# Kernel optimization log

Measured on AMD Instinct MI355X. Metric: run time of the kernel, lower is better.

Reference implementation:

```python
import jax, jax.numpy as jnp
import numpy as np

KMEANS_ITERS = 3   # soft-kmeans refinement iterations
TOPK = 12          # hardcoded in the torch module
EPS = 1e-8


def _gather(x, idx):
    # batched_index_select: x (b, c, m); idx (b, n, k) -> (b, c, n, k)
    return jax.vmap(lambda xb, ib: xb[:, ib])(x, idx)


def _soft_kmeans(points, cent):
    # points (b, n, c); cent (b, m, c) -> refined centroids and soft assignment weights (b, n, m)
    for _ in range(KMEANS_ITERS):
        p2 = jnp.sum(points * points, axis=-1)           # (b, n)
        c2 = jnp.sum(cent * cent, axis=-1)               # (b, m)
        logits = -(p2[:, :, None] - 2.0 * jnp.einsum('bnc,bmc->bnm', points, cent) + c2[:, None, :])
        w = jax.nn.softmax(logits, axis=-1)              # (b, n, m)
        cent = jnp.einsum('bnm,bnc->bmc', w, points) / (jnp.sum(w, axis=1)[:, :, None] + EPS)
    return cent, w


def setup_inputs():
    key = jax.random.key(0)
    k1, k2, k3 = jax.random.split(key, 3)
    b, c, H, W, k = 4, 192, 80, 80, 9
    n = H * W
    out_c = 192
    x = jax.random.normal(k1, (b, c, n, 1), dtype=jnp.float32)
    edge_index = jax.random.randint(k2, (2, b, n, k), 0, n)
    conv_w = jax.random.normal(k3, (out_c, 3 * c), dtype=jnp.float32) * (1.0 / np.sqrt(3 * c))
    conv_b = jnp.zeros((out_c,), dtype=jnp.float32)
    return {"x": x, "edge_index": edge_index, "conv_w": conv_w, "conv_b": conv_b,
            "num_centroids": 50, "H": 80, "W": 80}


def reference(x, edge_index, conv_w, conv_b, num_centroids, H, W):
    b, c, n, _ = x.shape
    xs = x[..., 0]                                        # (b, c, n)
    # initial centroids: adaptive_avg_pool2d to (5, 10); H, W chosen divisible so bins are uniform
    x_img = xs.reshape(b, c, H, W)
    init_cent = x_img.reshape(b, c, 5, H // 5, 10, W // 10).mean(axis=(3, 5)).reshape(b, c, 50)
    # edge gathers + max-relative reduction
    x_i = _gather(xs, edge_index[1])                      # (b, c, n, k)
    x_j = _gather(xs, edge_index[0])                      # (b, c, n, k)
    x_j = jnp.max(x_j - x_i, axis=-1, keepdims=True)      # (b, c, n, 1)
    # soft-kmeans centroid construction
    points = jnp.transpose(xs, (0, 2, 1))                 # (b, n, c)
    cent, weights = _soft_kmeans(points, jnp.transpose(init_cent, (0, 2, 1)))
    cent = jnp.transpose(cent, (0, 2, 1))                 # (b, c, m)
    # topk centroid routing + second gather-max stage
    _, nn_idx = jax.lax.top_k(weights, TOPK)              # (b, n, 12)
    x_jc = _gather(cent, nn_idx)                          # (b, c, n, 12)
    x_jc = jnp.max(x_jc - xs[..., None], axis=-1, keepdims=True)  # (b, c, n, 1)
    # channel-interleaved concat (matches torch stack on dim=2 then reshape to 3c)
    feat = jnp.stack([x, x_j, x_jc], axis=2).reshape(b, 3 * c, n)  # (b, 3c, n)
    # BasicConv: 1x1 conv + bias + relu (norm=None)
    out = jnp.einsum('oi,bin->bon', conv_w, feat) + conv_b[None, :, None]
    return jax.nn.relu(out)[..., None]                    # (b, out_c, n, 1)
```

## Files before the change

### kernel.cpp

```cpp
#include <hip/hip_runtime.h>
#include <hip/hip_bf16.h>
#include <math.h>

#define B_   4
#define C_   192
#define N_   6400
#define K_   9
#define M_   50
#define TK_  12
#define OC_  192
#define KC_  576
#define CH_  100
#define LSTR 53
#define TSTR 72
#define XSTR 40
#define GSTR 40

typedef __bf16 b16x8 __attribute__((ext_vector_type(8)));
typedef float f32x4 __attribute__((ext_vector_type(4)));

__device__ inline unsigned short f2b(float f) {
    union { __hip_bfloat16 h; unsigned short u; } v;
    v.h = __float2bfloat16(f);
    return v.u;
}
__device__ inline float b2f(unsigned short u) {
    union { float f; unsigned int i; } v;
    v.i = ((unsigned int)u) << 16;
    return v.f;
}

__global__ void k_rearrange_w(const float* __restrict__ cw, unsigned short* __restrict__ Wg16) {
    int g = blockIdx.x * 256 + threadIdx.x;
    int o = g / KC_, r = g % KC_;
    int t = r / C_, ch = r % C_;
    Wg16[g] = f2b(cw[o * KC_ + ch * 3 + t]);
}

__global__ void k_transpose(const float* __restrict__ x, float* __restrict__ xt,
                            unsigned short* __restrict__ xt16,
                            unsigned short* __restrict__ xt16l) {
    __shared__ float tile[32][33];
    int b = blockIdx.z;
    int p0 = blockIdx.x * 32, c0 = blockIdx.y * 32;
    int tx = threadIdx.x, ty = threadIdx.y;
    const float* xb = x + (size_t)b * C_ * N_;
    float* xtb = xt + (size_t)b * N_ * C_;
    unsigned short* xt16b = xt16 + (size_t)b * N_ * C_;
    unsigned short* xt16lb = xt16l + (size_t)b * N_ * C_;
#pragma unroll
    for (int i = 0; i < 4; i++) {
        int cc = ty + 8 * i;
        tile[cc][tx] = xb[(size_t)(c0 + cc) * N_ + p0 + tx];
    }
    __syncthreads();
#pragma unroll
    for (int i = 0; i < 4; i++) {
        int pp = ty + 8 * i;
        float v = tile[tx][pp];
        size_t o = (size_t)(p0 + pp) * C_ + c0 + tx;
        xtb[o] = v;
        unsigned short hi = f2b(v);
        xt16b[o] = hi;
        xt16lb[o] = f2b(v - b2f(hi));
    }
}

__global__ __launch_bounds__(192) void k_init_cent(const float* __restrict__ xt,
        float* __restrict__ cent, float* __restrict__ c2,
        unsigned short* __restrict__ centh, unsigned short* __restrict__ centl) {
    int m = blockIdx.x, b = blockIdx.y, c = threadIdx.x;
    if (m >= M_) {
        size_t o = ((size_t)b * 64 + m) * C_ + c;
        centh[o] = 0; centl[o] = 0;
        return;
    }
    int gy = m / 10, gx = m % 10;
    const float* xtb = xt + (size_t)b * N_ * C_;
    float s = 0.f;
    for (int yy = 0; yy < 16; yy++)
        for (int xx = 0; xx < 8; xx++) {
            int p = (gy * 16 + yy) * 80 + gx * 8 + xx;
            s += xtb[(size_t)p * C_ + c];
        }
    float v = s * (1.f / 128.f);
    cent[((size_t)b * M_ + m) * C_ + c] = v;
    size_t oh = ((size_t)b * 64 + m) * C_ + c;
    unsigned short hi = f2b(v);
    centh[oh] = hi;
    centl[oh] = f2b(v - b2f(hi));
    float q = v * v;
    __shared__ float red[3];
#pragma unroll
    for (int off = 32; off > 0; off >>= 1) q += __shfl_down(q, off, 64);
    if ((c & 63) == 0) red[c >> 6] = q;
    __syncthreads();
    if (c == 0) c2[(size_t)b * M_ + m] = red[0] + red[1] + red[2];
}

__global__ __launch_bounds__(256) void k_logits_upd(const float* __restrict__ xt,
        const unsigned short* __restrict__ xt16, const unsigned short* __restrict__ xt16l,
        const float* __restrict__ cent,
        const unsigned short* __restrict__ centh, const unsigned short* __restrict__ centl,
        const float* __restrict__ c2g,
        float* __restrict__ part, float* __restrict__ wsp,
        int* __restrict__ nn, int do_topk, int fast) {
    __shared__ alignas(16) char smem[51712];
    __shared__ float sred[256];
    float* Ac = (float*)smem;
    float* Bp = (float*)(smem + 4352);
    float* lg = (float*)(smem + 20480);
    unsigned short* lgTh = (unsigned short*)smem;
    unsigned short* lgTl = (unsigned short*)(smem + 9216);
    unsigned short* xTh = (unsigned short*)(smem + 18432);
    unsigned short* xTl = (unsigned short*)(smem + 35072);
    int b = blockIdx.y;
    int blk = blockIdx.x;
    int p0 = blk * 64;
    int tid = threadIdx.x;
    int tx = tid & 15, ty = tid >> 4;
    int lr = tid >> 2, lq = tid & 3;
    int wave = tid >> 6, lane = tid & 63;
    int m16 = lane & 15, q = lane >> 4;
    const float* xb = xt + ((size_t)b * N_ + p0) * C_;
    const unsigned short* x16b = xt16 + ((size_t)b * N_ + p0) * C_;
    const unsigned short* x16lb = xt16l + ((size_t)b * N_ + p0) * C_;
    if (fast) {
        const unsigned short* chg = centh + (size_t)b * 64 * C_;
        const unsigned short* clg = centl + (size_t)b * 64 * C_;
        f32x4 acc1[4];
#pragma unroll
        for (int i = 0; i < 4; i++) acc1[i] = (f32x4){0.f, 0.f, 0.f, 0.f};
#pragma unroll
        for (int kt = 0; kt < 6; kt++) {
            int kg = kt * 32;
            size_t xo = (size_t)(wave * 16 + m16) * C_ + kg + q * 8;
            b16x8 bh = *(const b16x8*)&x16b[xo];
            b16x8 bl = *(const b16x8*)&x16lb[xo];
#pragma unroll
            for (int mt = 0; mt < 4; mt++) {
                size_t co = (size_t)(mt * 16 + m16) * C_ + kg + q * 8;
                b16x8 ah = *(const b16x8*)&chg[co];
                b16x8 al = *(const b16x8*)&clg[co];
                acc1[mt] = __builtin_amdgcn_mfma_f32_16x16x32_bf16(ah, bh, acc1[mt], 0, 0, 0);
                acc1[mt] = __builtin_amdgcn_mfma_f32_16x16x32_bf16(ah, bl, acc1[mt], 0, 0, 0);
                acc1[mt] = __builtin_amdgcn_mfma_f32_16x16x32_bf16(al, bh, acc1[mt], 0, 0, 0);
            }
        }
#pragma unroll
        for (int mt = 0; mt < 4; mt++) {
#pragma unroll
            for (int r = 0; r < 4; r++) {
                int m = mt * 16 + q * 4 + r;
                if (m < M_) {
                    float c2v = c2g[(size_t)b * M_ + m];
                    lg[(wave * 16 + m16) * LSTR + m] = 2.f * acc1[mt][r] - c2v;
                }
            }
        }
    } else {
        const float* cb = cent + (size_t)b * M_ * C_;
        float acc[4][4];
#pragma unroll
        for (int i = 0; i < 4; i++)
#pragma unroll
            for (int j = 0; j < 4; j++) acc[i][j] = 0.f;
        for (int kt = 0; kt < 12; kt++) {
            int kg = kt * 16;
            float4 cv = make_float4(0.f, 0.f, 0.f, 0.f);
            if (lr < M_) cv = *(const float4*)&cb[(size_t)lr * C_ + kg + 4 * lq];
            float4 pv = *(const float4*)&xb[(size_t)lr * C_ + kg + 4 * lq];
            __syncthreads();
            Ac[(4 * lq + 0) * 68 + lr] = cv.x; Ac[(4 * lq + 1) * 68 + lr] = cv.y;
            Ac[(4 * lq + 2) * 68 + lr] = cv.z; Ac[(4 * lq + 3) * 68 + lr] = cv.w;
            Bp[(4 * lq + 0) * 68 + lr] = pv.x; Bp[(4 * lq + 1) * 68 + lr] = pv.y;
            Bp[(4 * lq + 2) * 68 + lr] = pv.z; Bp[(4 * lq + 3) * 68 + lr] = pv.w;
            __syncthreads();
#pragma unroll
            for (int kk = 0; kk < 16; kk++) {
                float4 a = *(const float4*)&Ac[kk * 68 + 4 * ty];
                float4 bb = *(const float4*)&Bp[kk * 68 + 4 * tx];
                acc[0][0] += a.x * bb.x; acc[0][1] += a.x * bb.y; acc[0][2] += a.x * bb.z; acc[0][3] += a.x * bb.w;
                acc[1][0] += a.y * bb.x; acc[1][1] += a.y * bb.y; acc[1][2] += a.y * bb.z; acc[1][3] += a.y * bb.w;
                acc[2][0] += a.z * bb.x; acc[2][1] += a.z * bb.y; acc[2][2] += a.z * bb.z; acc[2][3] += a.z * bb.w;
                acc[3][0] += a.w * bb.x; acc[3][1] += a.w * bb.y; acc[3][2] += a.w * bb.z; acc[3][3] += a.w * bb.w;
            }
        }
        __syncthreads();
#pragma unroll
        for (int i = 0; i < 4; i++) {
            int m = 4 * ty + i;
            if (m < M_) {
                float c2v = c2g[(size_t)b * M_ + m];
#pragma unroll
                for (int j = 0; j < 4; j++)
                    lg[(4 * tx + j) * LSTR + m] = 2.f * acc[i][j] - c2v;
            }
        }
    }
    __syncthreads();
    {
        int p = tid & 63, prt = tid >> 6;
        int m0 = prt * 13;
        int m1 = (prt == 3) ? M_ : m0 + 13;
        float* row = &lg[p * LSTR];
        float mx = -1e30f;
        for (int m = m0; m < m1; m++) mx = fmaxf(mx, row[m]);
        sred[prt * 64 + p] = mx;
        __syncthreads();
        mx = fmaxf(fmaxf(sred[p], sred[64 + p]), fmaxf(sred[128 + p], sred[192 + p]));
        float s = 0.f;
        for (int m = m0; m < m1; m++) {
            float e = expf(row[m] - mx);
            row[m] = e;
            s += e;
        }
        __syncthreads();
        sred[prt * 64 + p] = s;
        __syncthreads();
        s = sred[p] + sred[64 + p] + sred[128 + p] + sred[192 + p];
        float inv = 1.f / s;
        for (int m = m0; m < m1; m++) row[m] *= inv;
    }
    __syncthreads();
    for (int j = tid; j < 64 * 64; j += 256) {
        int m = j >> 6, p = j & 63;
        float w = (m < M_) ? lg[p * LSTR + m] : 0.f;
        unsigned short hi = f2b(w);
        lgTh[m * TSTR + p] = hi;
        lgTl[m * TSTR + p] = f2b(w - b2f(hi));
    }
    __syncthreads();
    if (do_topk && tid < 64) {
        float* row = &lg[tid * LSTR];
        int* nb = nn + ((size_t)b * N_ + p0 + tid) * TK_;
        for (int r = 0; r < TK_; r++) {
            float bv = -1.f;
            int bi = 0;
            for (int m = 0; m < M_; m++) {
                float v = row[m];
                if (v > bv) { bv = v; bi = m; }
            }
            nb[r] = bi;
            row[bi] = -1.f;
        }
    }
    f32x4 acc2[13];
#pragma unroll
    for (int i = 0; i < 13; i++) acc2[i] = (f32x4){0.f, 0.f, 0.f, 0.f};
    for (int h = 0; h < 2; h++) {
        __syncthreads();
        for (int j = tid; j < 32 * 24; j += 256) {
            int pl = j & 31, ko = (j >> 5) * 8;
            int4 vh = *(const int4*)&x16b[(size_t)(h * 32 + pl) * C_ + ko];
            int4 vl = *(const int4*)&x16lb[(size_t)(h * 32 + pl) * C_ + ko];
            const unsigned short* ph = (const unsigned short*)&vh;
            const unsigned short* pv = (const unsigned short*)&vl;
#pragma unroll
            for (int i = 0; i < 8; i++) {
                xTh[(ko + i) * XSTR + pl] = ph[i];
                xTl[(ko + i) * XSTR + pl] = pv[i];
            }
        }
        for (int j = tid; j < 32 * 16; j += 256) {
            int pl = j & 31, c = C_ + (j >> 5);
            xTh[c * XSTR + pl] = (c == C_) ? f2b(1.f) : 0;
            xTl[c * XSTR + pl] = 0;
        }
        __syncthreads();
        b16x8 ah = *(const b16x8*)&lgTh[(wave * 16 + m16) * TSTR + h * 32 + q * 8];
        b16x8 al = *(const b16x8*)&lgTl[(wave * 16 + m16) * TSTR + h * 32 + q * 8];
#pragma unroll
        for (int ct = 0; ct < 13; ct++) {
            b16x8 bh = *(const b16x8*)&xTh[(ct * 16 + m16) * XSTR + q * 8];
            b16x8 bl = *(const b16x8*)&xTl[(ct * 16 + m16) * XSTR + q * 8];
            acc2[ct] = __builtin_amdgcn_mfma_f32_16x16x32_bf16(ah, bh, acc2[ct], 0, 0, 0);
            acc2[ct] = __builtin_amdgcn_mfma_f32_16x16x32_bf16(ah, bl, acc2[ct], 0, 0, 0);
            acc2[ct] = __builtin_amdgcn_mfma_f32_16x16x32_bf16(al, bh, acc2[ct], 0, 0, 0);
        }
    }
    float* pb = part + ((size_t)b * CH_ + blk) * (size_t)(M_ * C_);
    int mbase = wave * 16 + q * 4;
#pragma unroll
    for (int ct = 0; ct < 13; ct++) {
        int c = ct * 16 + m16;
#pragma unroll
        for (int r = 0; r < 4; r++) {
            int mm = mbase + r;
            if (mm >= M_) continue;
            float v = acc2[ct][r];
            if (c < C_) pb[(size_t)mm * C_ + c] = v;
            else if (c == C_) wsp[((size_t)b * CH_ + blk) * M_ + mm] = v;
        }
    }
}

__global__ __launch_bounds__(192) void k_upd_reduce(const float* __restrict__ part,
        const float* __restrict__ wsp, float* __restrict__ cent, float* __restrict__ c2,
        unsigned short* __restrict__ cent16,
        unsigned short* __restrict__ centh, unsigned short* __restrict__ centl, int last) {
    int m = blockIdx.x, b = blockIdx.y, c = threadIdx.x;
    __shared__ float sws;
    __shared__ float red[3];
    if (c == 0) {
        float s = 0.f;
        for (int ch = 0; ch < CH_; ch++) s += wsp[((size_t)b * CH_ + ch) * M_ + m];
        sws = s + 1e-8f;
    }
    float s = 0.f;
    for (int ch = 0; ch < CH_; ch++)
        s += part[(((size_t)b * CH_ + ch) * M_ + m) * (size_t)C_ + c];
    __syncthreads();
    float v = s / sws;
    size_t o = ((size_t)b * M_ + m) * C_ + c;
    cent[o] = v;
    if (last) cent16[o] = f2b(v);
    size_t oh = ((size_t)b * 64 + m) * C_ + c;
    unsigned short hi = f2b(v);
    centh[oh] = hi;
    centl[oh] = f2b(v - b2f(hi));
    float q = v * v;
#pragma unroll
    for (int off = 32; off > 0; off >>= 1) q += __shfl_down(q, off, 64);
    if ((c & 63) == 0) red[c >> 6] = q;
    __syncthreads();
    if (c == 0) c2[(size_t)b * M_ + m] = red[0] + red[1] + red[2];
}

__global__ __launch_bounds__(192) void k_gather(const unsigned short* __restrict__ xt16,
        const unsigned short* __restrict__ cent16, const int* __restrict__ edge,
        const int* __restrict__ nn, unsigned short* __restrict__ xjt16,
        unsigned short* __restrict__ xjct16) {
    __shared__ int sidx[2 * K_ + TK_];
    int p = blockIdx.x, b = blockIdx.y, c = threadIdx.x;
    if (c < K_)
        sidx[c] = edge[((size_t)b * N_ + p) * K_ + c];
    else if (c < 2 * K_)
        sidx[c] = edge[(size_t)B_ * N_ * K_ + ((size_t)b * N_ + p) * K_ + (c - K_)];
    else if (c < 2 * K_ + TK_)
        sidx[c] = nn[((size_t)b * N_ + p) * TK_ + (c - 2 * K_)];
    __syncthreads();
    const unsigned short* xb = xt16 + (size_t)b * N_ * C_;
    const unsigned short* cbv = cent16 + (size_t)b * M_ * C_;
    float xv = b2f(xb[(size_t)p * C_ + c]);
    float mj = -1e30f;
#pragma unroll
    for (int kk = 0; kk < K_; kk++) {
        float vj = b2f(xb[(size_t)sidx[kk] * C_ + c]);
        float vi = b2f(xb[(size_t)sidx[K_ + kk] * C_ + c]);
        mj = fmaxf(mj, vj - vi);
    }
    float mc = -1e30f;
#pragma unroll
    for (int kk = 0; kk < TK_; kk++)
        mc = fmaxf(mc, b2f(cbv[(size_t)sidx[2 * K_ + kk] * C_ + c]));
    size_t o = ((size_t)b * N_ + p) * C_ + c;
    xjt16[o] = f2b(mj);
    xjct16[o] = f2b(mc - xv);
}

__global__ __launch_bounds__(256) void k_gemm(const unsigned short* __restrict__ Wg16,
        const unsigned short* __restrict__ xt16, const unsigned short* __restrict__ xjt16,
        const unsigned short* __restrict__ xjct16, const float* __restrict__ bias,
        float* __restrict__ out) {
    __shared__ short As[192 * GSTR];
    __shared__ short Bs[64 * GSTR];
    int b = blockIdx.y;
    int po = blockIdx.x * 64;
    int tid = threadIdx.x;
    int wave = tid >> 6, lane = tid & 63;
    int m16 = lane & 15, q = lane >> 4;
    const unsigned short* s0 = xt16 + (size_t)b * N_ * C_;
    const unsigned short* s1 = xjt16 + (size_t)b * N_ * C_;
    const unsigned short* s2 = xjct16 + (size_t)b * N_ * C_;
    f32x4 acc[12];
#pragma unroll
    for (int i = 0; i < 12; i++) acc[i] = (f32x4){0.f, 0.f, 0.f, 0.f};
    int brow = tid >> 2, bch = tid & 3;
    for (int kt = 0; kt < 18; kt++) {
        int kg = kt * 32;
        int prt = kg / C_, koff = kg - prt * C_;
        const unsigned short* src = (prt == 0) ? s0 : ((prt == 1) ? s1 : s2);
        int4 av[3];
#pragma unroll
        for (int t = 0; t < 3; t++) {
            int idx = t * 256 + tid;
            av[t] = *(const int4*)&Wg16[(size_t)(idx >> 2) * KC_ + kg + (idx & 3) * 8];
        }
        int4 bv = *(const int4*)&src[(size_t)(po + brow) * C_ + koff + bch * 8];
        __syncthreads();
#pragma unroll
        for (int t = 0; t < 3; t++) {
            int idx = t * 256 + tid;
            *(int4*)&As[(idx >> 2) * GSTR + (idx & 3) * 8] = av[t];
        }
        *(int4*)&Bs[brow * GSTR + bch * 8] = bv;
        __syncthreads();
        b16x8 bf = *(const b16x8*)&Bs[(wave * 16 + m16) * GSTR + q * 8];
#pragma unroll
        for (int of = 0; of < 12; of++) {
            b16x8 af = *(const b16x8*)&As[(of * 16 + m16) * GSTR + q * 8];
            acc[of] = __builtin_amdgcn_mfma_f32_16x16x32_bf16(af, bf, acc[of], 0, 0, 0);
        }
    }
    int p = po + wave * 16 + m16;
#pragma unroll
    for (int of = 0; of < 12; of++) {
        int o = of * 16 + q * 4;
        float4 bv = *(const float4*)&bias[o];
        float bia[4] = {bv.x, bv.y, bv.z, bv.w};
#pragma unroll
        for (int r = 0; r < 4; r++)
            out[((size_t)b * OC_ + o + r) * N_ + p] = fmaxf(acc[of][r] + bia[r], 0.f);
    }
}

extern "C" void kernel_launch(void* const* d_in, const int* in_sizes, int n_in,
                              void* d_out, int out_size, void* d_ws, size_t ws_size,
                              hipStream_t stream) {
    (void)in_sizes; (void)n_in; (void)out_size; (void)ws_size;
    const float* x   = (const float*)d_in[0];
    const int* edge  = (const int*)d_in[1];
    const float* cw  = (const float*)d_in[2];
    const float* cbi = (const float*)d_in[3];
    float* ws = (float*)d_ws;
    size_t o = 0;
    float* xt   = ws + o; o += (size_t)B_ * N_ * C_;
    unsigned short* xt16 = (unsigned short*)(ws + o); o += (size_t)B_ * N_ * C_ / 2;
    unsigned short* xt16l = (unsigned short*)(ws + o); o += (size_t)B_ * N_ * C_ / 2;
    unsigned short* Wg16 = (unsigned short*)(ws + o); o += (size_t)OC_ * KC_ / 2;
    float* cent = ws + o; o += (size_t)B_ * M_ * C_;
    unsigned short* cent16 = (unsigned short*)(ws + o); o += (size_t)B_ * M_ * C_ / 2;
    unsigned short* centh = (unsigned short*)(ws + o); o += (size_t)B_ * 64 * C_ / 2;
    unsigned short* centl = (unsigned short*)(ws + o); o += (size_t)B_ * 64 * C_ / 2;
    float* c2   = ws + o; o += (size_t)B_ * M_;
    float* part = ws + o; o += (size_t)B_ * CH_ * M_ * C_;
    float* wsp  = ws + o; o += (size_t)B_ * CH_ * M_;
    int* nn = (int*)(ws + o); o += (size_t)B_ * N_ * TK_;
    unsigned short* xjt16  = (unsigned short*)(ws + o); o += (size_t)B_ * N_ * C_ / 2;
    unsigned short* xjct16 = (unsigned short*)(ws + o); o += (size_t)B_ * N_ * C_ / 2;
    float* outp = (float*)d_out;

    k_rearrange_w<<<dim3(432), dim3(256), 0, stream>>>(cw, Wg16);
    k_transpose<<<dim3(N_ / 32, C_ / 32, B_), dim3(32, 8), 0, stream>>>(x, xt, xt16, xt16l);
    k_init_cent<<<dim3(64, B_), dim3(192), 0, stream>>>(xt, cent, c2, centh, centl);
    for (int it = 0; it < 3; it++) {
        k_logits_upd<<<dim3(CH_, B_), dim3(256), 0, stream>>>(xt, xt16, xt16l, cent,
            centh, centl, c2, part, wsp, nn, (it == 2) ? 1 : 0, (it < 2) ? 1 : 0);
        k_upd_reduce<<<dim3(M_, B_), dim3(192), 0, stream>>>(part, wsp, cent, c2,
            cent16, centh, centl, (it == 2) ? 1 : 0);
    }
    k_gather<<<dim3(N_, B_), dim3(192), 0, stream>>>(xt16, cent16, edge, nn, xjt16, xjct16);
    k_gemm<<<dim3(N_ / 64, B_), dim3(256), 0, stream>>>(Wg16, xt16, xjt16, xjct16, cbi, outp);
}
```

Baseline: 293.8 us.

## Halve point chunk per block in logits/centroid-update kernel to double grid size

Changes the per-block point tile in the soft-kmeans logits/update kernel from 64 to 32 points, doubling the number of blocks (CH_ 100→200). The MFMA work is redistributed across waves, the softmax reduction uses 8 partitions of 32 points, and the centroid accumulation does a single 32-point K pass instead of two. Shared memory is also cut to about 43 KB. This aims to raise occupancy and parallelism, at the cost of twice as many partial-sum buffers for the later reduction and less work per block.

```diff
diff --git a/kernel.cpp b/kernel.cpp
--- a/kernel.cpp
+++ b/kernel.cpp
@@ -10,10 +10,10 @@
 #define TK_  12
 #define OC_  192
 #define KC_  576
-#define CH_  100
+#define CH_  200
+#define PC_  32
 #define LSTR 53
-#define TSTR 72
-#define XSTR 40
+#define TSTR 40
 #define GSTR 40
 
 typedef __bf16 b16x8 __attribute__((ext_vector_type(8)));
@@ -105,18 +105,18 @@
         const float* __restrict__ c2g,
         float* __restrict__ part, float* __restrict__ wsp,
         int* __restrict__ nn, int do_topk, int fast) {
-    __shared__ alignas(16) char smem[51712];
+    __shared__ alignas(16) char smem[43520];
     __shared__ float sred[256];
     float* Ac = (float*)smem;
     float* Bp = (float*)(smem + 4352);
-    float* lg = (float*)(smem + 20480);
-    unsigned short* lgTh = (unsigned short*)smem;
-    unsigned short* lgTl = (unsigned short*)(smem + 9216);
-    unsigned short* xTh = (unsigned short*)(smem + 18432);
-    unsigned short* xTl = (unsigned short*)(smem + 35072);
+    float* lg = (float*)(smem + 6656);
+    unsigned short* xTh = (unsigned short*)smem;
+    unsigned short* xTl = (unsigned short*)(smem + 16640);
+    unsigned short* lgTh = (unsigned short*)(smem + 33280);
+    unsigned short* lgTl = (unsigned short*)(smem + 38400);
     int b = blockIdx.y;
     int blk = blockIdx.x;
-    int p0 = blk * 64;
+    int p0 = blk * PC_;
     int tid = threadIdx.x;
     int tx = tid & 15, ty = tid >> 4;
     int lr = tid >> 2, lq = tid & 3;
@@ -128,62 +128,67 @@
     if (fast) {
         const unsigned short* chg = centh + (size_t)b * 64 * C_;
         const unsigned short* clg = centl + (size_t)b * 64 * C_;
-        f32x4 acc1[4];
-#pragma unroll
-        for (int i = 0; i < 4; i++) acc1[i] = (f32x4){0.f, 0.f, 0.f, 0.f};
+        int pt = wave & 1, mt0 = wave >> 1;
+        f32x4 acc1[2];
+        acc1[0] = (f32x4){0.f, 0.f, 0.f, 0.f};
+        acc1[1] = (f32x4){0.f, 0.f, 0.f, 0.f};
 #pragma unroll
         for (int kt = 0; kt < 6; kt++) {
             int kg = kt * 32;
-            size_t xo = (size_t)(wave * 16 + m16) * C_ + kg + q * 8;
+            size_t xo = (size_t)(pt * 16 + m16) * C_ + kg + q * 8;
             b16x8 bh = *(const b16x8*)&x16b[xo];
             b16x8 bl = *(const b16x8*)&x16lb[xo];
 #pragma unroll
-            for (int mt = 0; mt < 4; mt++) {
+            for (int i = 0; i < 2; i++) {
+                int mt = mt0 + 2 * i;
                 size_t co = (size_t)(mt * 16 + m16) * C_ + kg + q * 8;
                 b16x8 ah = *(const b16x8*)&chg[co];
                 b16x8 al = *(const b16x8*)&clg[co];
-                acc1[mt] = __builtin_amdgcn_mfma_f32_16x16x32_bf16(ah, bh, acc1[mt], 0, 0, 0);
-                acc1[mt] = __builtin_amdgcn_mfma_f32_16x16x32_bf16(ah, bl, acc1[mt], 0, 0, 0);
-                acc1[mt] = __builtin_amdgcn_mfma_f32_16x16x32_bf16(al, bh, acc1[mt], 0, 0, 0);
-            }
-        }
-#pragma unroll
-        for (int mt = 0; mt < 4; mt++) {
+                acc1[i] = __builtin_amdgcn_mfma_f32_16x16x32_bf16(ah, bh, acc1[i], 0, 0, 0);
+                acc1[i] = __builtin_amdgcn_mfma_f32_16x16x32_bf16(ah, bl, acc1[i], 0, 0, 0);
+                acc1[i] = __builtin_amdgcn_mfma_f32_16x16x32_bf16(al, bh, acc1[i], 0, 0, 0);
+            }
+        }
+#pragma unroll
+        for (int i = 0; i < 2; i++) {
+            int mt = mt0 + 2 * i;
 #pragma unroll
             for (int r = 0; r < 4; r++) {
                 int m = mt * 16 + q * 4 + r;
                 if (m < M_) {
                     float c2v = c2g[(size_t)b * M_ + m];
-                    lg[(wave * 16 + m16) * LSTR + m] = 2.f * acc1[mt][r] - c2v;
+                    lg[(pt * 16 + m16) * LSTR + m] = 2.f * acc1[i][r] - c2v;
                 }
             }
         }
     } else {
         const float* cb = cent + (size_t)b * M_ * C_;
-        float acc[4][4];
-#pragma unroll
-        for (int i = 0; i < 4; i++)
-#pragma unroll
-            for (int j = 0; j < 4; j++) acc[i][j] = 0.f;
+        float acc[4][2];
+#pragma unroll
+        for (int i = 0; i < 4; i++) { acc[i][0] = 0.f; acc[i][1] = 0.f; }
         for (int kt = 0; kt < 12; kt++) {
             int kg = kt * 16;
             float4 cv = make_float4(0.f, 0.f, 0.f, 0.f);
             if (lr < M_) cv = *(const float4*)&cb[(size_t)lr * C_ + kg + 4 * lq];
-            float4 pv = *(const float4*)&xb[(size_t)lr * C_ + kg + 4 * lq];
+            float4 pv = make_float4(0.f, 0.f, 0.f, 0.f);
+            if (tid < 128) pv = *(const float4*)&xb[(size_t)(tid >> 2) * C_ + kg + 4 * lq];
             __syncthreads();
             Ac[(4 * lq + 0) * 68 + lr] = cv.x; Ac[(4 * lq + 1) * 68 + lr] = cv.y;
             Ac[(4 * lq + 2) * 68 + lr] = cv.z; Ac[(4 * lq + 3) * 68 + lr] = cv.w;
-            Bp[(4 * lq + 0) * 68 + lr] = pv.x; Bp[(4 * lq + 1) * 68 + lr] = pv.y;
-            Bp[(4 * lq + 2) * 68 + lr] = pv.z; Bp[(4 * lq + 3) * 68 + lr] = pv.w;
+            if (tid < 128) {
+                int xr = tid >> 2;
+                Bp[(4 * lq + 0) * 36 + xr] = pv.x; Bp[(4 * lq + 1) * 36 + xr] = pv.y;
+                Bp[(4 * lq + 2) * 36 + xr] = pv.z; Bp[(4 * lq + 3) * 36 + xr] = pv.w;
+            }
             __syncthreads();
 #pragma unroll
             for (int kk = 0; kk < 16; kk++) {
                 float4 a = *(const float4*)&Ac[kk * 68 + 4 * ty];
-                float4 bb = *(const float4*)&Bp[kk * 68 + 4 * tx];
-                acc[0][0] += a.x * bb.x; acc[0][1] += a.x * bb.y; acc[0][2] += a.x * bb.z; acc[0][3] += a.x * bb.w;
-                acc[1][0] += a.y * bb.x; acc[1][1] += a.y * bb.y; acc[1][2] += a.y * bb.z; acc[1][3] += a.y * bb.w;
-                acc[2][0] += a.z * bb.x; acc[2][1] += a.z * bb.y; acc[2][2] += a.z * bb.z; acc[2][3] += a.z * bb.w;
-                acc[3][0] += a.w * bb.x; acc[3][1] += a.w * bb.y; acc[3][2] += a.w * bb.z; acc[3][3] += a.w * bb.w;
+                float2 bb = *(const float2*)&Bp[kk * 36 + 2 * tx];
+                acc[0][0] += a.x * bb.x; acc[0][1] += a.x * bb.y;
+                acc[1][0] += a.y * bb.x; acc[1][1] += a.y * bb.y;
+                acc[2][0] += a.z * bb.x; acc[2][1] += a.z * bb.y;
+                acc[3][0] += a.w * bb.x; acc[3][1] += a.w * bb.y;
             }
         }
         __syncthreads();
@@ -192,23 +197,24 @@
             int m = 4 * ty + i;
             if (m < M_) {
                 float c2v = c2g[(size_t)b * M_ + m];
-#pragma unroll
-                for (int j = 0; j < 4; j++)
-                    lg[(4 * tx + j) * LSTR + m] = 2.f * acc[i][j] - c2v;
+                lg[(2 * tx + 0) * LSTR + m] = 2.f * acc[i][0] - c2v;
+                lg[(2 * tx + 1) * LSTR + m] = 2.f * acc[i][1] - c2v;
             }
         }
     }
     __syncthreads();
     {
-        int p = tid & 63, prt = tid >> 6;
-        int m0 = prt * 13;
-        int m1 = (prt == 3) ? M_ : m0 + 13;
+        int p = tid & 31, prt = tid >> 5;
+        int m0 = prt * 6;
+        int m1 = (prt == 7) ? M_ : m0 + 6;
         float* row = &lg[p * LSTR];
         float mx = -1e30f;
         for (int m = m0; m < m1; m++) mx = fmaxf(mx, row[m]);
-        sred[prt * 64 + p] = mx;
-        __syncthreads();
-        mx = fmaxf(fmaxf(sred[p], sred[64 + p]), fmaxf(sred[128 + p], sred[192 + p]));
+        sred[prt * 32 + p] = mx;
+        __syncthreads();
+        mx = sred[p];
+#pragma unroll
+        for (int k = 1; k < 8; k++) mx = fmaxf(mx, sred[k * 32 + p]);
         float s = 0.f;
         for (int m = m0; m < m1; m++) {
             float e = expf(row[m] - mx);
@@ -216,22 +222,24 @@
             s += e;
         }
         __syncthreads();
-        sred[prt * 64 + p] = s;
-        __syncthreads();
-        s = sred[p] + sred[64 + p] + sred[128 + p] + sred[192 + p];
+        sred[prt * 32 + p] = s;
+        __syncthreads();
+        s = sred[p];
+#pragma unroll
+        for (int k = 1; k < 8; k++) s += sred[k * 32 + p];
         float inv = 1.f / s;
         for (int m = m0; m < m1; m++) row[m] *= inv;
     }
     __syncthreads();
-    for (int j = tid; j < 64 * 64; j += 256) {
-        int m = j >> 6, p = j & 63;
+    for (int j = tid; j < 64 * PC_; j += 256) {
+        int m = j >> 5, p = j & 31;
         float w = (m < M_) ? lg[p * LSTR + m] : 0.f;
         unsigned short hi = f2b(w);
         lgTh[m * TSTR + p] = hi;
         lgTl[m * TSTR + p] = f2b(w - b2f(hi));
     }
     __syncthreads();
-    if (do_topk && tid < 64) {
+    if (do_topk && tid < PC_) {
         float* row = &lg[tid * LSTR];
         int* nb = nn + ((size_t)b * N_ + p0 + tid) * TK_;
         for (int r = 0; r < TK_; r++) {
@@ -245,35 +253,35 @@
             row[bi] = -1.f;
         }
     }
+    __syncthreads();
+    for (int j = tid; j < PC_ * 24; j += 256) {
+        int pl = j & 31, ko = (j >> 5) * 8;
+        int4 vh = *(const int4*)&x16b[(size_t)pl * C_ + ko];
+        int4 vl = *(const int4*)&x16lb[(size_t)pl * C_ + ko];
+        const unsigned short* ph = (const unsigned short*)&vh;
+        const unsigned short* pv = (const unsigned short*)&vl;
+#pragma unroll
+        for (int i = 0; i < 8; i++) {
+            xTh[(ko + i) * TSTR + pl] = ph[i];
+            xTl[(ko + i) * TSTR + pl] = pv[i];
+        }
+    }
+    for (int j = tid; j < PC_ * 16; j += 256) {
+        int pl = j & 31, c = C_ + (j >> 5);
+        xTh[c * TSTR + pl] = (c == C_) ? f2b(1.f) : 0;
+        xTl[c * TSTR + pl] = 0;
+    }
+    __syncthreads();
     f32x4 acc2[13];
 #pragma unroll
     for (int i = 0; i < 13; i++) acc2[i] = (f32x4){0.f, 0.f, 0.f, 0.f};
-    for (int h = 0; h < 2; h++) {
-        __syncthreads();
-        for (int j = tid; j < 32 * 24; j += 256) {
-            int pl = j & 31, ko = (j >> 5) * 8;
-            int4 vh = *(const int4*)&x16b[(size_t)(h * 32 + pl) * C_ + ko];
-            int4 vl = *(const int4*)&x16lb[(size_t)(h * 32 + pl) * C_ + ko];
-            const unsigned short* ph = (const unsigned short*)&vh;
-            const unsigned short* pv = (const unsigned short*)&vl;
-#pragma unroll
-            for (int i = 0; i < 8; i++) {
-                xTh[(ko + i) * XSTR + pl] = ph[i];
-                xTl[(ko + i) * XSTR + pl] = pv[i];
-            }
-        }
-        for (int j = tid; j < 32 * 16; j += 256) {
-            int pl = j & 31, c = C_ + (j >> 5);
-            xTh[c * XSTR + pl] = (c == C_) ? f2b(1.f) : 0;
-            xTl[c * XSTR + pl] = 0;
-        }
-        __syncthreads();
-        b16x8 ah = *(const b16x8*)&lgTh[(wave * 16 + m16) * TSTR + h * 32 + q * 8];
-        b16x8 al = *(const b16x8*)&lgTl[(wave * 16 + m16) * TSTR + h * 32 + q * 8];
+    {
+        b16x8 ah = *(const b16x8*)&lgTh[(wave * 16 + m16) * TSTR + q * 8];
+        b16x8 al = *(const b16x8*)&lgTl[(wave * 16 + m16) * TSTR + q * 8];
 #pragma unroll
         for (int ct = 0; ct < 13; ct++) {
-            b16x8 bh = *(const b16x8*)&xTh[(ct * 16 + m16) * XSTR + q * 8];
-            b16x8 bl = *(const b16x8*)&xTl[(ct * 16 + m16) * XSTR + q * 8];
+            b16x8 bh = *(const b16x8*)&xTh[(ct * 16 + m16) * TSTR + q * 8];
+            b16x8 bl = *(const b16x8*)&xTl[(ct * 16 + m16) * TSTR + q * 8];
             acc2[ct] = __builtin_amdgcn_mfma_f32_16x16x32_bf16(ah, bh, acc2[ct], 0, 0, 0);
             acc2[ct] = __builtin_amdgcn_mfma_f32_16x16x32_bf16(ah, bl, acc2[ct], 0, 0, 0);
             acc2[ct] = __builtin_amdgcn_mfma_f32_16x16x32_bf16(al, bh, acc2[ct], 0, 0, 0);
```

New measurement: 365.3 us. 24.4% more time.
